# Kernel optimization log

Hardware: AMD Instinct MI355X
Metric: run time of the kernel (lower is better)

Reference implementation:

```python
import jax, jax.numpy as jnp
import numpy as np
import math

B, N, DIN, DH, DOUT = 32, 4096, 2, 512, 3
L = 3                      # num_hidden_modulation_matrices = num_layers - 2
LAT, MH, R = 512, 512, 5   # latent_dim, modulation_net_dim_hidden, UV_rank
W0, W0I = 30.0, 30.0
UV_END = 2 * DH * R * L
MOD_OUT = UV_END + DOUT * DH


def setup_inputs() -> dict:
    key = jax.random.key(0)
    ks = jax.random.split(key, 14)
    def unif(k, shape, s):
        return jax.random.uniform(k, shape, jnp.float32, -s, s)
    s0 = 1.0 / DIN                      # SIREN first-layer init bound
    sh = math.sqrt(6.0 / DH) / W0       # sqrt(c/dim_in)/w0 with c=6
    return {
        "x": jax.random.uniform(ks[0], (B, N, DIN), jnp.float32),
        "latent": jax.random.normal(ks[1], (B, LAT), jnp.float32),
        "W0": unif(ks[2], (DH, DIN), s0), "b0": unif(ks[3], (DH,), s0),
        "Wh": unif(ks[4], (L, DH, DH), sh), "bh": unif(ks[5], (L, DH), sh),
        "Wlast": unif(ks[6], (DOUT, DH), sh), "blast": unif(ks[7], (DOUT,), sh),
        "ln_g": jnp.ones((LAT,), jnp.float32), "ln_b": jnp.zeros((LAT,), jnp.float32),
        "Wm_in": jax.random.normal(ks[8], (MH, LAT), jnp.float32) * 0.02,
        "bm_in": jnp.zeros((MH,), jnp.float32),
        "Wr1": jax.random.normal(ks[9], (2, MH, MH), jnp.float32) * 0.02,
        "br1": jnp.zeros((2, MH), jnp.float32),
        "Wr2": jax.random.normal(ks[10], (2, MH, MH), jnp.float32) * 0.02,
        "br2": jnp.zeros((2, MH), jnp.float32),
        "Wm_out": jax.random.normal(ks[11], (MOD_OUT, MH), jnp.float32) * 0.02,
        "bm_out": jnp.zeros((MOD_OUT,), jnp.float32),
    }


def _modulation_net(latent, ln_g, ln_b, Wm_in, bm_in, Wr1, br1, Wr2, br2, Wm_out, bm_out):
    # LayerNorm(latent)
    mu = jnp.mean(latent, axis=-1, keepdims=True)
    var = jnp.var(latent, axis=-1, keepdims=True)
    h = (latent - mu) / jnp.sqrt(var + 1e-5) * ln_g + ln_b
    h = jax.nn.leaky_relu(h @ Wm_in.T + bm_in)
    for i in range(2):  # ResBlocks (use_batch_norm=False path)
        t = jax.nn.leaky_relu(h @ Wr1[i].T + br1[i])
        t = t @ Wr2[i].T + br2[i]
        h = jax.nn.leaky_relu(h + t)
    out = h @ Wm_out.T + bm_out                      # (B, MOD_OUT)
    UV = out[:, :UV_END].reshape(B, L, 2, DH, R)
    U, V = UV[:, :, 0], UV[:, :, 1]                  # (B, L, DH, R) each
    last_mod = jax.nn.sigmoid(out[:, UV_END:].reshape(B, DOUT, DH))
    return U, V, last_mod


def _forward(x, latent, W0_, b0, Wh, bh, Wlast, blast,
             ln_g, ln_b, Wm_in, bm_in, Wr1, br1, Wr2, br2, Wm_out, bm_out):
    U, V, last_mod = _modulation_net(latent, ln_g, ln_b, Wm_in, bm_in,
                                     Wr1, br1, Wr2, br2, Wm_out, bm_out)
    # first (unmodulated) SIREN layer
    h = jnp.sin(W0I * (x @ W0_.T + b0))              # (B, N, DH)
    # modulated hidden layers: per-sample low-rank weight scaling
    for i in range(L):
        G = jax.nn.sigmoid(jnp.einsum('bhr,bir->bhi', U[:, i], V[:, i]))  # (B, DH, DH)
        h = jnp.einsum('bni,bhi->bnh', h, (G + 1.0) * Wh[i]) + bh[i]
        h = jnp.sin(W0 * h)
    # modulated last layer (is_last: +0.5, no activation)
    out = jnp.einsum('bni,boi->bno', h, last_mod * Wlast) + blast + 0.5
    return out


def reference(x, latent, W0, b0, Wh, bh, Wlast, blast,
              ln_g, ln_b, Wm_in, bm_in, Wr1, br1, Wr2, br2, Wm_out, bm_out):
    return _forward(x, latent, W0, b0, Wh, bh, Wlast, blast,
                    ln_g, ln_b, Wm_in, bm_in, Wr1, br1, Wr2, br2, Wm_out, bm_out)
```

## Files before the change

kernel.cpp:

```cpp
#include <hip/hip_runtime.h>

#define UV_END_ 15360
#define MODOUT_ 16896

typedef __attribute__((ext_vector_type(8))) short s8v;
typedef __attribute__((ext_vector_type(4))) short s4v;
typedef __attribute__((ext_vector_type(8))) __bf16 bf16x8;
typedef __attribute__((ext_vector_type(4))) float f4v;

static __device__ __forceinline__ unsigned short f2bf(float f) {
  unsigned u = __float_as_uint(f);
  u += 0x7fffu + ((u >> 16) & 1u);
  return (unsigned short)(u >> 16);
}
static __device__ __forceinline__ float bf2f(unsigned short s) {
  return __uint_as_float(((unsigned)s) << 16);
}


__global__ void k_ln(const float* __restrict__ latent, const float* __restrict__ g,
                     const float* __restrict__ bb, float* __restrict__ nrm) {
  __shared__ float rs[256], rq[256];
  int b = blockIdx.x, t = threadIdx.x;
  float a0 = latent[b * 512 + t], a1 = latent[b * 512 + t + 256];
  rs[t] = a0 + a1; rq[t] = a0 * a0 + a1 * a1;
  __syncthreads();
  for (int k = 128; k > 0; k >>= 1) {
    if (t < k) { rs[t] += rs[t + k]; rq[t] += rq[t + k]; }
    __syncthreads();
  }
  float mean = rs[0] * (1.0f / 512.0f);
  float var = rq[0] * (1.0f / 512.0f) - mean * mean;
  float rstd = rsqrtf(var + 1e-5f);
  nrm[b * 512 + t]       = (a0 - mean) * rstd * g[t] + bb[t];
  nrm[b * 512 + t + 256] = (a1 - mean) * rstd * g[t + 256] + bb[t + 256];
}

__global__ void k_modlin(const float* __restrict__ hin, const float* __restrict__ W,
                         const float* __restrict__ bias, const float* __restrict__ res,
                         float* __restrict__ hout) {
  __shared__ float hs[512];
  int b = blockIdx.y, t = threadIdx.x;
  hs[t] = hin[b * 512 + t];
  hs[t + 256] = hin[b * 512 + t + 256];
  __syncthreads();
  int o = blockIdx.x * 256 + t;
  const f4v* wr = (const f4v*)(W + (size_t)o * 512);
  float acc = bias[o];
  #pragma unroll 8
  for (int c = 0; c < 128; ++c) {
    f4v w = wr[c];
    acc += w.x * hs[c * 4] + w.y * hs[c * 4 + 1] + w.z * hs[c * 4 + 2] + w.w * hs[c * 4 + 3];
  }
  if (res) acc += res[b * 512 + o];
  hout[b * 512 + o] = acc > 0.f ? acc : 0.01f * acc;
}

__global__ void k_modout(const float* __restrict__ h, const float* __restrict__ Wm,
                         const float* __restrict__ bm, const float* __restrict__ Wlast,
                         float* __restrict__ modout, float* __restrict__ Wfin) {
  int t = threadIdx.x;
  int o = blockIdx.x * 8 + (t >> 5);
  int b = t & 31;
  const f4v* wr = (const f4v*)(Wm + (size_t)o * 512);
  const f4v* hr = (const f4v*)(h + b * 512);
  float acc = bm[o];
  #pragma unroll 4
  for (int c = 0; c < 128; ++c) {
    f4v w = wr[c], v = hr[c];
    acc += w.x * v.x + w.y * v.y + w.z * v.z + w.w * v.w;
  }
  if (o < UV_END_) {
    modout[(size_t)b * MODOUT_ + o] = acc;
  } else {
    int r = o - UV_END_;
    int od = r >> 9, hh = r & 511;
    float s = 1.f / (1.f + __expf(-acc));
    Wfin[(b * 3 + od) * 512 + hh] = s * Wlast[od * 512 + hh];
  }
}

__global__ void k_wprep(const float* __restrict__ modout, const float* __restrict__ Wh,
                        unsigned short* __restrict__ Wmod) {
  __shared__ float Vs[2560];
  __shared__ float Us[320];
  int ht = blockIdx.x, l = blockIdx.y, b = blockIdx.z, t = threadIdx.x;
  const float* mo = modout + (size_t)b * MODOUT_ + l * 5120;
  for (int i = t; i < 2560; i += 256) Vs[i] = mo[2560 + i];
  for (int i = t; i < 320; i += 256) Us[i] = mo[ht * 320 + i];
  __syncthreads();
  int hl = t >> 2;
  int h = ht * 64 + hl;
  float u0 = Us[hl * 5], u1 = Us[hl * 5 + 1], u2 = Us[hl * 5 + 2],
        u3 = Us[hl * 5 + 3], u4 = Us[hl * 5 + 4];
  const float* whr = Wh + ((size_t)(l * 512 + h)) * 512;
  unsigned short* wmr = Wmod + (((size_t)(b * 3 + l)) * 512 + h) * 512;
  for (int c = 0; c < 16; ++c) {
    int i0 = (t & 3) * 128 + c * 8;
    s8v pk;
    #pragma unroll
    for (int j = 0; j < 8; ++j) {
      int i = i0 + j;
      float gg = u0 * Vs[i * 5] + u1 * Vs[i * 5 + 1] + u2 * Vs[i * 5 + 2]
               + u3 * Vs[i * 5 + 3] + u4 * Vs[i * 5 + 4];
      float sg = 1.f / (1.f + __expf(-gg));
      float m = (sg + 1.f) * whr[i];
      pk[j] = (short)f2bf(m);
    }
    *(s8v*)(wmr + i0) = pk;
  }
}

__global__ __launch_bounds__(256, 2) void k_main(
    const float* __restrict__ x, const float* __restrict__ W0w,
    const float* __restrict__ b0, const unsigned short* __restrict__ Wmod,
    const float* __restrict__ bh, const float* __restrict__ Wfin,
    const float* __restrict__ blast, float* __restrict__ out) {
  __shared__ unsigned short hlds[64 * 512];
  const int b = blockIdx.y, tile = blockIdx.x, t = threadIdx.x;
  const int lane = t & 63, wv = t >> 6;
  const int n0 = tile * 64;

  {
    int n = t >> 2;
    float x0 = x[((size_t)b * 4096 + n0 + n) * 2 + 0];
    float x1 = x[((size_t)b * 4096 + n0 + n) * 2 + 1];
    int swz = (n & 7) << 3;
    for (int c = 0; c < 16; ++c) {
      int i0 = (t & 3) * 128 + c * 8;
      s8v pk;
      #pragma unroll
      for (int j = 0; j < 8; ++j) {
        int i = i0 + j;
        float pre = x0 * W0w[i * 2] + x1 * W0w[i * 2 + 1] + b0[i];
        pk[j] = (short)f2bf(__sinf(30.0f * pre));
      }
      *(s8v*)&hlds[n * 512 + (i0 ^ swz)] = pk;
    }
  }
  __syncthreads();

  const int arow = lane & 15;
  const int kgrp = (lane >> 4) * 8;
  const int hbase = wv * 128;

  for (int l = 0; l < 3; ++l) {
    const unsigned short* wp = Wmod + (((size_t)b * 3 + l) << 18)
                             + (size_t)(hbase + arow) * 512 + kgrp;
    f4v acc[8][4];
    #pragma unroll
    for (int fi = 0; fi < 8; ++fi)
      #pragma unroll
      for (int fj = 0; fj < 4; ++fj) { f4v z = {0.f, 0.f, 0.f, 0.f}; acc[fi][fj] = z; }

    s8v abuf0[8], abuf1[8];
    #pragma unroll
    for (int fi = 0; fi < 8; ++fi) abuf0[fi] = *(const s8v*)(wp + fi * 16 * 512);

    #pragma unroll 1
    for (int ks = 0; ks < 16; ks += 2) {
      {
        #pragma unroll
        for (int fi = 0; fi < 8; ++fi)
          abuf1[fi] = *(const s8v*)(wp + fi * 16 * 512 + (ks + 1) * 32);
        int icol = ks * 32 + kgrp;
        bf16x8 bv[4];
        #pragma unroll
        for (int fj = 0; fj < 4; ++fj) {
          int n = fj * 16 + arow;
          bv[fj] = __builtin_bit_cast(bf16x8,
                     *(const s8v*)&hlds[n * 512 + (icol ^ ((n & 7) << 3))]);
        }
        #pragma unroll
        for (int fi = 0; fi < 8; ++fi) {
          bf16x8 av = __builtin_bit_cast(bf16x8, abuf0[fi]);
          #pragma unroll
          for (int fj = 0; fj < 4; ++fj)
            acc[fi][fj] = __builtin_amdgcn_mfma_f32_16x16x32_bf16(av, bv[fj], acc[fi][fj], 0, 0, 0);
        }
      }
      {
        int ks2 = (ks + 2 < 16) ? (ks + 2) : 14;
        #pragma unroll
        for (int fi = 0; fi < 8; ++fi)
          abuf0[fi] = *(const s8v*)(wp + fi * 16 * 512 + ks2 * 32);
        int icol = (ks + 1) * 32 + kgrp;
        bf16x8 bv[4];
        #pragma unroll
        for (int fj = 0; fj < 4; ++fj) {
          int n = fj * 16 + arow;
          bv[fj] = __builtin_bit_cast(bf16x8,
                     *(const s8v*)&hlds[n * 512 + (icol ^ ((n & 7) << 3))]);
        }
        #pragma unroll
        for (int fi = 0; fi < 8; ++fi) {
          bf16x8 av = __builtin_bit_cast(bf16x8, abuf1[fi]);
          #pragma unroll
          for (int fj = 0; fj < 4; ++fj)
            acc[fi][fj] = __builtin_amdgcn_mfma_f32_16x16x32_bf16(av, bv[fj], acc[fi][fj], 0, 0, 0);
        }
      }
    }
    __syncthreads();

    const float* bhp = bh + l * 512;
    #pragma unroll
    for (int fi = 0; fi < 8; ++fi) {
      int hh = hbase + fi * 16 + (lane >> 4) * 4;
      float bv0 = bhp[hh], bv1 = bhp[hh + 1], bv2 = bhp[hh + 2], bv3 = bhp[hh + 3];
      #pragma unroll
      for (int fj = 0; fj < 4; ++fj) {
        int n = fj * 16 + arow;
        f4v a = acc[fi][fj];
        s4v pk;
        pk[0] = (short)f2bf(__sinf(30.f * (a.x + bv0)));
        pk[1] = (short)f2bf(__sinf(30.f * (a.y + bv1)));
        pk[2] = (short)f2bf(__sinf(30.f * (a.z + bv2)));
        pk[3] = (short)f2bf(__sinf(30.f * (a.w + bv3)));
        *(s4v*)&hlds[n * 512 + (hh ^ ((n & 7) << 3))] = pk;
      }
    }
    __syncthreads();
  }

  if (t < 192) {
    int n = t / 3, o = t - n * 3;
    const f4v* wf = (const f4v*)(Wfin + ((size_t)b * 3 + o) * 512);
    int swz = (n & 7) << 3;
    float acc = 0.f;
    #pragma unroll 4
    for (int c = 0; c < 64; ++c) {
      int i0 = c * 8;
      s8v hv = *(const s8v*)&hlds[n * 512 + (i0 ^ swz)];
      f4v w0 = wf[c * 2], w1 = wf[c * 2 + 1];
      acc += bf2f((unsigned short)hv[0]) * w0.x + bf2f((unsigned short)hv[1]) * w0.y
           + bf2f((unsigned short)hv[2]) * w0.z + bf2f((unsigned short)hv[3]) * w0.w
           + bf2f((unsigned short)hv[4]) * w1.x + bf2f((unsigned short)hv[5]) * w1.y
           + bf2f((unsigned short)hv[6]) * w1.z + bf2f((unsigned short)hv[7]) * w1.w;
    }
    out[((size_t)b * 4096 + n0 + n) * 3 + o] = acc + blast[o] + 0.5f;
  }
}

extern "C" void kernel_launch(void* const* d_in, const int* in_sizes, int n_in,
                              void* d_out, int out_size, void* d_ws, size_t ws_size,
                              hipStream_t stream) {
  const float* x      = (const float*)d_in[0];
  const float* latent = (const float*)d_in[1];
  const float* W0w    = (const float*)d_in[2];
  const float* b0     = (const float*)d_in[3];
  const float* Wh     = (const float*)d_in[4];
  const float* bh     = (const float*)d_in[5];
  const float* Wlast  = (const float*)d_in[6];
  const float* blast  = (const float*)d_in[7];
  const float* ln_g   = (const float*)d_in[8];
  const float* ln_b   = (const float*)d_in[9];
  const float* Wm_in  = (const float*)d_in[10];
  const float* bm_in  = (const float*)d_in[11];
  const float* Wr1    = (const float*)d_in[12];
  const float* br1    = (const float*)d_in[13];
  const float* Wr2    = (const float*)d_in[14];
  const float* br2    = (const float*)d_in[15];
  const float* Wm_out = (const float*)d_in[16];
  const float* bm_out = (const float*)d_in[17];
  float* out = (float*)d_out;

  float* nrm    = (float*)d_ws;
  float* h1     = nrm + 32 * 512;
  float* h2     = h1 + 32 * 512;
  float* tb     = h2 + 32 * 512;
  float* modout = tb + 32 * 512;
  float* Wfin   = modout + (size_t)32 * MODOUT_;
  unsigned short* Wmod = (unsigned short*)(Wfin + 32 * 3 * 512);

  k_ln<<<32, 256, 0, stream>>>(latent, ln_g, ln_b, nrm);
  k_modlin<<<dim3(2, 32), 256, 0, stream>>>(nrm, Wm_in, bm_in, nullptr, h1);
  k_modlin<<<dim3(2, 32), 256, 0, stream>>>(h1, Wr1, br1, nullptr, tb);
  k_modlin<<<dim3(2, 32), 256, 0, stream>>>(tb, Wr2, br2, h1, h2);
  k_modlin<<<dim3(2, 32), 256, 0, stream>>>(h2, Wr1 + 512 * 512, br1 + 512, nullptr, tb);
  k_modlin<<<dim3(2, 32), 256, 0, stream>>>(tb, Wr2 + 512 * 512, br2 + 512, h2, h1);
  k_modout<<<2112, 256, 0, stream>>>(h1, Wm_out, bm_out, Wlast, modout, Wfin);
  k_wprep<<<dim3(8, 3, 32), 256, 0, stream>>>(modout, Wh, Wmod);
  k_main<<<dim3(64, 32), 256, 0, stream>>>(x, W0w, b0, Wmod, bh, Wfin, blast, out);
}
```

Before: 911.0 us.

## Fuse modulation MLP into one kernel and retile main kernel with XCD-aware mapping

Replaces the LayerNorm kernel and five per-layer linear launches with a single per-sample kernel that keeps activations in shared memory, cutting launch count and global round-trips. The main kernel now uses 512 threads per block (8 waves, each owning 64 output rows) and maps a 1D grid so that each XCD handles a contiguous set of batch samples, improving L2 reuse of the per-sample modulated weights. It also raises MFMA issue priority around the inner loops. The fused modnet runs only 32 blocks, so each block performs 2.5M MACs serially, which may make that stage slower than the spread-out launches.

```diff
diff --git a/kernel.cpp b/kernel.cpp
--- a/kernel.cpp
+++ b/kernel.cpp
@@ -17,43 +17,89 @@
   return __uint_as_float(((unsigned)s) << 16);
 }
 
-
-__global__ void k_ln(const float* __restrict__ latent, const float* __restrict__ g,
-                     const float* __restrict__ bb, float* __restrict__ nrm) {
-  __shared__ float rs[256], rq[256];
-  int b = blockIdx.x, t = threadIdx.x;
-  float a0 = latent[b * 512 + t], a1 = latent[b * 512 + t + 256];
-  rs[t] = a0 + a1; rq[t] = a0 * a0 + a1 * a1;
-  __syncthreads();
-  for (int k = 128; k > 0; k >>= 1) {
-    if (t < k) { rs[t] += rs[t + k]; rq[t] += rq[t + k]; }
-    __syncthreads();
-  }
-  float mean = rs[0] * (1.0f / 512.0f);
-  float var = rq[0] * (1.0f / 512.0f) - mean * mean;
-  float rstd = rsqrtf(var + 1e-5f);
-  nrm[b * 512 + t]       = (a0 - mean) * rstd * g[t] + bb[t];
-  nrm[b * 512 + t + 256] = (a1 - mean) * rstd * g[t + 256] + bb[t + 256];
-}
-
-__global__ void k_modlin(const float* __restrict__ hin, const float* __restrict__ W,
-                         const float* __restrict__ bias, const float* __restrict__ res,
-                         float* __restrict__ hout) {
-  __shared__ float hs[512];
-  int b = blockIdx.y, t = threadIdx.x;
-  hs[t] = hin[b * 512 + t];
-  hs[t + 256] = hin[b * 512 + t + 256];
-  __syncthreads();
-  int o = blockIdx.x * 256 + t;
-  const f4v* wr = (const f4v*)(W + (size_t)o * 512);
-  float acc = bias[o];
+static __device__ __forceinline__ float dot512(const float* __restrict__ W,
+                                               const float* __restrict__ hs) {
+  const f4v* wr = (const f4v*)W;
+  float acc = 0.f;
   #pragma unroll 8
   for (int c = 0; c < 128; ++c) {
     f4v w = wr[c];
     acc += w.x * hs[c * 4] + w.y * hs[c * 4 + 1] + w.z * hs[c * 4 + 2] + w.w * hs[c * 4 + 3];
   }
-  if (res) acc += res[b * 512 + o];
-  hout[b * 512 + o] = acc > 0.f ? acc : 0.01f * acc;
+  return acc;
+}
+
+__global__ __launch_bounds__(256) void k_modnet(
+    const float* __restrict__ latent, const float* __restrict__ ln_g,
+    const float* __restrict__ ln_b,
+    const float* __restrict__ Wm_in, const float* __restrict__ bm_in,
+    const float* __restrict__ Wr1, const float* __restrict__ br1,
+    const float* __restrict__ Wr2, const float* __restrict__ br2,
+    float* __restrict__ hout) {
+  __shared__ float A[512], B_[512], C[512];
+  __shared__ float red[34];
+  int b = blockIdx.x, t = threadIdx.x;
+  float a0 = latent[b * 512 + t], a1 = latent[b * 512 + t + 256];
+  float s = a0 + a1, q = a0 * a0 + a1 * a1;
+  #pragma unroll
+  for (int off = 32; off > 0; off >>= 1) {
+    s += __shfl_down(s, off);
+    q += __shfl_down(q, off);
+  }
+  int wv = t >> 6, ln = t & 63;
+  if (ln == 0) { red[wv] = s; red[8 + wv] = q; }
+  __syncthreads();
+  if (t == 0) {
+    float ss = red[0] + red[1] + red[2] + red[3];
+    float qq = red[8] + red[9] + red[10] + red[11];
+    float mean = ss * (1.0f / 512.0f);
+    float var = qq * (1.0f / 512.0f) - mean * mean;
+    red[32] = mean;
+    red[33] = rsqrtf(var + 1e-5f);
+  }
+  __syncthreads();
+  float mean = red[32], rstd = red[33];
+  A[t]       = (a0 - mean) * rstd * ln_g[t] + ln_b[t];
+  A[t + 256] = (a1 - mean) * rstd * ln_g[t + 256] + ln_b[t + 256];
+  __syncthreads();
+
+  #pragma unroll
+  for (int p = 0; p < 2; ++p) {
+    int o = t + p * 256;
+    float acc = bm_in[o] + dot512(Wm_in + (size_t)o * 512, A);
+    B_[o] = acc > 0.f ? acc : 0.01f * acc;
+  }
+  __syncthreads();
+
+  #pragma unroll
+  for (int p = 0; p < 2; ++p) {
+    int o = t + p * 256;
+    float acc = br1[o] + dot512(Wr1 + (size_t)o * 512, B_);
+    C[o] = acc > 0.f ? acc : 0.01f * acc;
+  }
+  __syncthreads();
+  #pragma unroll
+  for (int p = 0; p < 2; ++p) {
+    int o = t + p * 256;
+    float acc = B_[o] + br2[o] + dot512(Wr2 + (size_t)o * 512, C);
+    A[o] = acc > 0.f ? acc : 0.01f * acc;
+  }
+  __syncthreads();
+
+  #pragma unroll
+  for (int p = 0; p < 2; ++p) {
+    int o = t + p * 256;
+    float acc = br1[512 + o] + dot512(Wr1 + 512 * 512 + (size_t)o * 512, A);
+    C[o] = acc > 0.f ? acc : 0.01f * acc;
+  }
+  __syncthreads();
+  #pragma unroll
+  for (int p = 0; p < 2; ++p) {
+    int o = t + p * 256;
+    float acc = A[o] + br2[512 + o] + dot512(Wr2 + 512 * 512 + (size_t)o * 512, C);
+    float r = acc > 0.f ? acc : 0.01f * acc;
+    hout[b * 512 + o] = r;
+  }
 }
 
 __global__ void k_modout(const float* __restrict__ h, const float* __restrict__ Wm,
@@ -111,23 +157,28 @@
   }
 }
 
-__global__ __launch_bounds__(256, 2) void k_main(
+__global__ __launch_bounds__(512, 4) void k_main(
     const float* __restrict__ x, const float* __restrict__ W0w,
     const float* __restrict__ b0, const unsigned short* __restrict__ Wmod,
     const float* __restrict__ bh, const float* __restrict__ Wfin,
     const float* __restrict__ blast, float* __restrict__ out) {
   __shared__ unsigned short hlds[64 * 512];
-  const int b = blockIdx.y, tile = blockIdx.x, t = threadIdx.x;
+  const int bid = blockIdx.x;
+  const int xcd = bid & 7, idx = bid >> 3;
+  const int b = xcd * 4 + (idx >> 6);
+  const int tile = idx & 63;
+  const int t = threadIdx.x;
   const int lane = t & 63, wv = t >> 6;
   const int n0 = tile * 64;
 
   {
-    int n = t >> 2;
+    int n = t >> 3;
     float x0 = x[((size_t)b * 4096 + n0 + n) * 2 + 0];
     float x1 = x[((size_t)b * 4096 + n0 + n) * 2 + 1];
     int swz = (n & 7) << 3;
-    for (int c = 0; c < 16; ++c) {
-      int i0 = (t & 3) * 128 + c * 8;
+    int cbase = (t & 7) * 64;
+    for (int c = 0; c < 8; ++c) {
+      int i0 = cbase + c * 8;
       s8v pk;
       #pragma unroll
       for (int j = 0; j < 8; ++j) {
@@ -142,26 +193,26 @@
 
   const int arow = lane & 15;
   const int kgrp = (lane >> 4) * 8;
-  const int hbase = wv * 128;
+  const int hbase = wv * 64;
 
   for (int l = 0; l < 3; ++l) {
-    const unsigned short* wp = Wmod + (((size_t)b * 3 + l) << 18)
+    const unsigned short* wp = Wmod + (((size_t)(b * 3 + l)) << 18)
                              + (size_t)(hbase + arow) * 512 + kgrp;
-    f4v acc[8][4];
+    f4v acc[4][4];
     #pragma unroll
-    for (int fi = 0; fi < 8; ++fi)
+    for (int fi = 0; fi < 4; ++fi)
       #pragma unroll
       for (int fj = 0; fj < 4; ++fj) { f4v z = {0.f, 0.f, 0.f, 0.f}; acc[fi][fj] = z; }
 
-    s8v abuf0[8], abuf1[8];
+    s8v abuf0[4], abuf1[4];
     #pragma unroll
-    for (int fi = 0; fi < 8; ++fi) abuf0[fi] = *(const s8v*)(wp + fi * 16 * 512);
+    for (int fi = 0; fi < 4; ++fi) abuf0[fi] = *(const s8v*)(wp + fi * 16 * 512);
 
     #pragma unroll 1
     for (int ks = 0; ks < 16; ks += 2) {
       {
         #pragma unroll
-        for (int fi = 0; fi < 8; ++fi)
+        for (int fi = 0; fi < 4; ++fi)
           abuf1[fi] = *(const s8v*)(wp + fi * 16 * 512 + (ks + 1) * 32);
         int icol = ks * 32 + kgrp;
         bf16x8 bv[4];
@@ -171,18 +222,20 @@
           bv[fj] = __builtin_bit_cast(bf16x8,
                      *(const s8v*)&hlds[n * 512 + (icol ^ ((n & 7) << 3))]);
         }
-        #pragma unroll
-        for (int fi = 0; fi < 8; ++fi) {
+        __builtin_amdgcn_s_setprio(1);
+        #pragma unroll
+        for (int fi = 0; fi < 4; ++fi) {
           bf16x8 av = __builtin_bit_cast(bf16x8, abuf0[fi]);
           #pragma unroll
           for (int fj = 0; fj < 4; ++fj)
             acc[fi][fj] = __builtin_amdgcn_mfma_f32_16x16x32_bf16(av, bv[fj], acc[fi][fj], 0, 0, 0);
         }
+        __builtin_amdgcn_s_setprio(0);
       }
       {
         int ks2 = (ks + 2 < 16) ? (ks + 2) : 14;
         #pragma unroll
-        for (int fi = 0; fi < 8; ++fi)
+        for (int fi = 0; fi < 4; ++fi)
           abuf0[fi] = *(const s8v*)(wp + fi * 16 * 512 + ks2 * 32);
         int icol = (ks + 1) * 32 + kgrp;
         bf16x8 bv[4];
@@ -192,20 +245,22 @@
           bv[fj] = __builtin_bit_cast(bf16x8,
                      *(const s8v*)&hlds[n * 512 + (icol ^ ((n & 7) << 3))]);
         }
-        #pragma unroll
-        for (int fi = 0; fi < 8; ++fi) {
+        __builtin_amdgcn_s_setprio(1);
+        #pragma unroll
+        for (int fi = 0; fi < 4; ++fi) {
           bf16x8 av = __builtin_bit_cast(bf16x8, abuf1[fi]);
           #pragma unroll
           for (int fj = 0; fj < 4; ++fj)
             acc[fi][fj] = __builtin_amdgcn_mfma_f32_16x16x32_bf16(av, bv[fj], acc[fi][fj], 0, 0, 0);
         }
+        __builtin_amdgcn_s_setprio(0);
       }
     }
     __syncthreads();
 
     const float* bhp = bh + l * 512;
     #pragma unroll
-    for (int fi = 0; fi < 8; ++fi) {
+    for (int fi = 0; fi < 4; ++fi) {
       int hh = hbase + fi * 16 + (lane >> 4) * 4;
       float bv0 = bhp[hh], bv1 = bhp[hh + 1], bv2 = bhp[hh + 2], bv3 = bhp[hh + 3];
       #pragma unroll
@@ -225,7 +280,7 @@
 
   if (t < 192) {
     int n = t / 3, o = t - n * 3;
-    const f4v* wf = (const f4v*)(Wfin + ((size_t)b * 3 + o) * 512);
+    const f4v* wf = (const f4v*)(Wfin + ((size_t)(b * 3 + o)) * 512);
     int swz = (n & 7) << 3;
     float acc = 0.f;
     #pragma unroll 4
@@ -265,21 +320,14 @@
   const float* bm_out = (const float*)d_in[17];
   float* out = (float*)d_out;
 
-  float* nrm    = (float*)d_ws;
-  float* h1     = nrm + 32 * 512;
-  float* h2     = h1 + 32 * 512;
-  float* tb     = h2 + 32 * 512;
-  float* modout = tb + 32 * 512;
+  float* h1     = (float*)d_ws;
+  float* modout = h1 + 32 * 512;
   float* Wfin   = modout + (size_t)32 * MODOUT_;
   unsigned short* Wmod = (unsigned short*)(Wfin + 32 * 3 * 512);
 
-  k_ln<<<32, 256, 0, stream>>>(latent, ln_g, ln_b, nrm);
-  k_modlin<<<dim3(2, 32), 256, 0, stream>>>(nrm, Wm_in, bm_in, nullptr, h1);
-  k_modlin<<<dim3(2, 32), 256, 0, stream>>>(h1, Wr1, br1, nullptr, tb);
-  k_modlin<<<dim3(2, 32), 256, 0, stream>>>(tb, Wr2, br2, h1, h2);
-  k_modlin<<<dim3(2, 32), 256, 0, stream>>>(h2, Wr1 + 512 * 512, br1 + 512, nullptr, tb);
-  k_modlin<<<dim3(2, 32), 256, 0, stream>>>(tb, Wr2 + 512 * 512, br2 + 512, h2, h1);
+  k_modnet<<<32, 256, 0, stream>>>(latent, ln_g, ln_b, Wm_in, bm_in,
+                                   Wr1, br1, Wr2, br2, h1);
   k_modout<<<2112, 256, 0, stream>>>(h1, Wm_out, bm_out, Wlast, modout, Wfin);
   k_wprep<<<dim3(8, 3, 32), 256, 0, stream>>>(modout, Wh, Wmod);
-  k_main<<<dim3(64, 32), 256, 0, stream>>>(x, W0w, b0, Wmod, bh, Wfin, blast, out);
-}
+  k_main<<<2048, 512, 0, stream>>>(x, W0w, b0, Wmod, bh, Wfin, blast, out);
+}
```

After: 987.3 us. 1.08x slower.
